# Kernel optimization log

Measured on AMD Instinct MI355X. Metric: run time of the kernel, lower is better.

The kernel has to match this reference:

```python
import jax, jax.numpy as jnp
import numpy as np

N_TRACKS = 2048          # chunk_size = 32*32*2 in the source
CONF_THRESHOLD = 3.0     # conf_threshold default
NORM_INLIER_THRESH = 0.01  # reprojection inlier threshold in normalized camera coords
PIX_THRESH = 1.5         # frame-0 pixel reprojection threshold from the source
MIN_TRI_INLIER = 4       # min_tri_inlier_num default


def setup_inputs() -> dict:
    key = jax.random.key(0)
    k1, k2, k3 = jax.random.split(key, 3)
    S, H, W = 8, 224, 224
    pts = jax.random.normal(k1, (S, H, W, 3), dtype=jnp.float32)
    # confidences in (1, 5) so (conf - 3 + 0.5) weights span negative/positive as in the source
    conf = 1.0 + 4.0 * jax.random.uniform(k2, (S, H, W), dtype=jnp.float32)
    K = jnp.array([[300.0, 0.0, W / 2.0], [0.0, 300.0, H / 2.0], [0.0, 0.0, 1.0]], dtype=jnp.float32)
    intrinsics = jnp.tile(K[None], (S, 1, 1))
    w2cs = jnp.tile(jnp.eye(4, dtype=jnp.float32)[None], (S, 1, 1))
    w2cs = w2cs.at[:, :3, 3].set(0.1 * jax.random.normal(k3, (S, 3), dtype=jnp.float32))
    return {"pts": pts, "conf": conf, "intrinsics": intrinsics, "w2cs": w2cs}


def reference(pts, conf, intrinsics, w2cs):
    S, H, W, _ = pts.shape
    HW = H * W
    pts_flat = pts.reshape(S, HW, 3)
    conf_flat = conf.reshape(S, HW)

    # --- sample N reference points in frame 0 by confidence (fixed-size analogue of quantile mask) ---
    _, idx0 = jax.lax.top_k(conf_flat[0], N_TRACKS)          # [N]
    ref = pts_flat[0, idx0]                                   # [N,3]
    ref_sq = (ref ** 2).sum(-1)                               # [N]

    # --- brute-force pairwise sq-dist + argmin match, per frame (memory-bound core) ---
    def match(frame_pts):  # frame_pts: [HW,3]
        d = ref_sq[:, None] - 2.0 * (ref @ frame_pts.T) + (frame_pts ** 2).sum(-1)[None, :]  # [N,HW]
        return jnp.argmin(d, axis=1)

    matches_rest = jax.lax.map(match, pts_flat[1:])           # [S-1,N]
    matches = jnp.concatenate([idx0[None], matches_rest], 0)  # [S,N]

    xs = (matches % W).astype(pts.dtype)
    ys = (matches // W).astype(pts.dtype)
    track_xy = jnp.stack([xs, ys], -1)                        # [S,N,2] (x,y) per source reorder [...,[1,0]]
    track_conf = jnp.take_along_axis(conf_flat, matches, axis=1)  # [S,N]

    # --- normalize tracks by intrinsics ---
    pp = intrinsics[:, :2, 2][:, None, :]                     # [S,1,2]
    f = jnp.stack([intrinsics[:, 0, 0], intrinsics[:, 1, 1]], -1)[:, None, :]  # [S,1,2]
    tn = (track_xy - pp) / f                                  # [S,N,2]

    # --- weighted multi-view DLT triangulation (conf-weighted, per-point 4x4 eigh) ---
    wgt = track_conf - CONF_THRESHOLD + 0.5                   # [S,N]
    P = w2cs[:, :3, :]                                        # [S,3,4]
    r1 = (tn[..., 0:1] * P[:, None, 2, :] - P[:, None, 0, :]) * wgt[..., None]  # [S,N,4]
    r2 = (tn[..., 1:2] * P[:, None, 2, :] - P[:, None, 1, :]) * wgt[..., None]
    AtA = jnp.einsum('sni,snj->nij', r1, r1) + jnp.einsum('sni,snj->nij', r2, r2)  # [N,4,4]
    _, evecs = jnp.linalg.eigh(AtA)
    v = evecs[..., 0]                                         # eigvec of smallest eigval, [N,4]
    denom = jnp.where(jnp.abs(v[:, 3:4]) < 1e-8, 1e-8, v[:, 3:4])
    X = v[:, :3] / denom                                      # [N,3] triangulated points

    # --- per-view reprojection, inlier count ---
    Xc = jnp.einsum('sij,nj->sni', P[:, :, :3], X) + P[:, None, :, 3]  # [S,N,3]
    z = Xc[..., 2:3]
    z = jnp.where(jnp.abs(z) < 1e-6, 1e-6, z)
    uv = Xc[..., :2] / z                                      # [S,N,2] normalized
    err = jnp.linalg.norm(uv - tn, axis=-1)                   # [S,N]
    inlier = err < NORM_INLIER_THRESH                         # [S,N]
    inlier_num = inlier.sum(0)                                # [N] int32

    # --- frame-0 pixel reprojection mask (source: (pos - track_matches[0]).norm < 1.5 & inlier_num > S//2) ---
    pos = uv[0] * f[0] + pp[0]                                # [N,2] pixels
    err_px0 = jnp.linalg.norm(pos - track_xy[0], axis=-1)
    final_mask = (err_px0 < PIX_THRESH) & (inlier_num > S // 2)

    # --- points_conf as in batched_triangulate ---
    pconf = (track_conf * inlier).sum(0) / jnp.clip(inlier_num, 1)
    pconf = jnp.where(inlier_num >= MIN_TRI_INLIER, pconf, 1.0)

    return X, pconf, final_mask.astype(jnp.int32), inlier_num
```

## Files before the change

kernel.cpp:

```cpp
#include <hip/hip_runtime.h>
#include <math.h>

#define HW       50176
#define W_IMG    224
#define S_FRAMES 8
#define NT       2048
#define NJCH     28
#define JCH      1792

__device__ unsigned           g_hist1[65536];
__device__ unsigned           g_hist2[65536];
__device__ unsigned           g_scalars[16];
__device__ unsigned long long g_keys[4096];
__device__ int                g_matches[S_FRAMES * NT];
__device__ float4             g_ref[NT];
__device__ float              g_pd[7 * NT * NJCH];
__device__ int                g_pj[7 * NT * NJCH];

__device__ __forceinline__ unsigned ordered_u32(float f) {
  unsigned u = __float_as_uint(f);
  return (u & 0x80000000u) ? ~u : (u | 0x80000000u);
}

__global__ void zero_kernel() {
  int i = blockIdx.x * blockDim.x + threadIdx.x;
  if (i < 65536) { g_hist1[i] = 0u; g_hist2[i] = 0u; }
  if (i < 4096)  g_keys[i] = 0ULL;
  if (i < 16)    g_scalars[i] = 0u;
}

__global__ void hist1_kernel(const float* __restrict__ conf) {
  int i = blockIdx.x * blockDim.x + threadIdx.x;
  if (i < HW) atomicAdd(&g_hist1[ordered_u32(conf[i]) >> 16], 1u);
}

__global__ void scan1_kernel() {
  __shared__ unsigned csum[256];
  __shared__ unsigned suf[256];
  int t = threadIdx.x;
  unsigned s = 0;
  for (int b = 0; b < 256; ++b) s += g_hist1[t * 256 + b];
  csum[t] = s;
  __syncthreads();
  if (t == 0) { unsigned run = 0; for (int c = 255; c >= 0; --c) { suf[c] = run; run += csum[c]; } }
  __syncthreads();
  unsigned run = suf[t];
  for (int b = 255; b >= 0; --b) {
    unsigned h = g_hist1[t * 256 + b];
    if (run < NT && run + h >= NT) { g_scalars[0] = (unsigned)(t * 256 + b); g_scalars[1] = run; }
    run += h;
  }
}

__global__ void hist2_kernel(const float* __restrict__ conf) {
  int i = blockIdx.x * blockDim.x + threadIdx.x;
  if (i < HW) {
    unsigned ou = ordered_u32(conf[i]);
    if ((ou >> 16) == g_scalars[0]) atomicAdd(&g_hist2[ou & 0xFFFFu], 1u);
  }
}

__global__ void scan2_kernel() {
  __shared__ unsigned csum[256];
  __shared__ unsigned suf[256];
  int t = threadIdx.x;
  unsigned R = NT - g_scalars[1];
  unsigned s = 0;
  for (int b = 0; b < 256; ++b) s += g_hist2[t * 256 + b];
  csum[t] = s;
  __syncthreads();
  if (t == 0) { unsigned run = 0; for (int c = 255; c >= 0; --c) { suf[c] = run; run += csum[c]; } }
  __syncthreads();
  unsigned run = suf[t];
  for (int b = 255; b >= 0; --b) {
    unsigned h = g_hist2[t * 256 + b];
    if (run < R && run + h >= R) g_scalars[2] = (g_scalars[0] << 16) | (unsigned)(t * 256 + b);
    run += h;
  }
}

__global__ void compact_kernel(const float* __restrict__ conf) {
  int i = blockIdx.x * blockDim.x + threadIdx.x;
  if (i < HW) {
    unsigned ou = ordered_u32(conf[i]);
    if (ou >= g_scalars[2]) {
      unsigned pos = atomicAdd(&g_scalars[4], 1u);
      if (pos < 4096) g_keys[pos] = ((unsigned long long)ou << 32) | (unsigned long long)(0xFFFFFFFFu - (unsigned)i);
    }
  }
}

__global__ __launch_bounds__(1024) void sortwrite_kernel(const float* __restrict__ pts) {
  __shared__ unsigned long long sk[4096];
  int t = threadIdx.x;
  for (int i = t; i < 4096; i += 1024) sk[i] = ~g_keys[i];
  for (unsigned k = 2; k <= 4096; k <<= 1) {
    for (unsigned j = k >> 1; j > 0; j >>= 1) {
      __syncthreads();
      for (unsigned i = t; i < 4096; i += 1024) {
        unsigned ixj = i ^ j;
        if (ixj > i) {
          unsigned long long a = sk[i], b = sk[ixj];
          bool up = ((i & k) == 0);
          if (up ? (a > b) : (a < b)) { sk[i] = b; sk[ixj] = a; }
        }
      }
    }
  }
  __syncthreads();
  for (int i = t; i < NT; i += 1024) {
    unsigned long long key = ~sk[i];
    unsigned idx = 0xFFFFFFFFu - (unsigned)(key & 0xFFFFFFFFu);
    g_matches[i] = (int)idx;
    const float* p = pts + (size_t)idx * 3;
    float x = p[0], y = p[1], z = p[2];
    g_ref[i] = make_float4(x, y, z, fmaf(x, x, fmaf(y, y, z * z)));
  }
}

__global__ __launch_bounds__(256) void match_kernel(const float* __restrict__ pts) {
  __shared__ float4 tile[256];
  int jc = blockIdx.x;
  int ic = blockIdx.y;
  int f  = blockIdx.z;
  int t  = threadIdx.x;
  int i  = ic * 256 + t;
  float4 r = g_ref[i];
  float dmin = INFINITY;
  int   jmin = 0;
  const float* fp = pts + (size_t)(f + 1) * HW * 3;
  int jbase0 = jc * JCH;
  for (int ti = 0; ti < 7; ++ti) {
    int jb = jbase0 + ti * 256;
    const float* p = fp + (size_t)(jb + t) * 3;
    float x = p[0], y = p[1], z = p[2];
    float sq = fmaf(x, x, fmaf(y, y, z * z));
    __syncthreads();
    tile[t] = make_float4(x, y, z, sq);
    __syncthreads();
#pragma unroll 8
    for (int u = 0; u < 256; ++u) {
      float4 q = tile[u];
      float dot = fmaf(q.x, r.x, fmaf(q.y, r.y, q.z * r.z));
      float d   = fmaf(-2.0f, dot, r.w) + q.w;
      if (d < dmin) { dmin = d; jmin = jb + u; }
    }
  }
  int id = f * NT + i;
  g_pd[id * NJCH + jc] = dmin;
  g_pj[id * NJCH + jc] = jmin;
}

__global__ void reduce_kernel() {
  int id = blockIdx.x * blockDim.x + threadIdx.x;
  if (id >= 7 * NT) return;
  float dmin = INFINITY;
  int   jmin = 0;
  for (int c = 0; c < NJCH; ++c) {
    float d = g_pd[id * NJCH + c];
    int   j = g_pj[id * NJCH + c];
    if (d < dmin) { dmin = d; jmin = j; }
  }
  int f = id / NT, i = id % NT;
  g_matches[(f + 1) * NT + i] = jmin;
}

__global__ void solve_kernel(const float* __restrict__ conf, const float* __restrict__ intr,
                             const float* __restrict__ w2cs, float* __restrict__ out) {
  int i = blockIdx.x * blockDim.x + threadIdx.x;
  if (i >= NT) return;

  float A1[10] = {0}, A2[10] = {0};
  float tnx[8], tny[8], cf[8];
  float x0 = 0.f, y0 = 0.f;

  for (int s = 0; s < S_FRAMES; ++s) {
    int m = g_matches[s * NT + i];
    float xs = (float)(m % W_IMG);
    float ys = (float)(m / W_IMG);
    float c  = conf[s * HW + m];
    float fx = intr[s * 9 + 0], fy = intr[s * 9 + 4];
    float cx = intr[s * 9 + 2], cy = intr[s * 9 + 5];
    float tx = (xs - cx) / fx;
    float ty = (ys - cy) / fy;
    float w  = (c - 3.0f) + 0.5f;
    const float* P = w2cs + s * 16;
    float r1[4], r2[4];
#pragma unroll
    for (int k = 0; k < 4; ++k) {
      r1[k] = (tx * P[8 + k] - P[k])     * w;
      r2[k] = (ty * P[8 + k] - P[4 + k]) * w;
    }
    int idx = 0;
#pragma unroll
    for (int a = 0; a < 4; ++a)
#pragma unroll
      for (int b = a; b < 4; ++b) {
        A1[idx] += r1[a] * r1[b];
        A2[idx] += r2[a] * r2[b];
        ++idx;
      }
    tnx[s] = tx; tny[s] = ty; cf[s] = c;
    if (s == 0) { x0 = xs; y0 = ys; }
  }

  double a[4][4], V[4][4];
  {
    int idx = 0;
#pragma unroll
    for (int p = 0; p < 4; ++p)
#pragma unroll
      for (int q = p; q < 4; ++q) {
        double v = (double)(A1[idx] + A2[idx]);
        a[p][q] = v; a[q][p] = v; ++idx;
      }
#pragma unroll
    for (int p = 0; p < 4; ++p)
#pragma unroll
      for (int q = 0; q < 4; ++q) V[p][q] = (p == q) ? 1.0 : 0.0;
  }

  for (int sweep = 0; sweep < 8; ++sweep) {
#pragma unroll
    for (int p = 0; p < 3; ++p)
#pragma unroll
      for (int q = p + 1; q < 4; ++q) {
        double apq = a[p][q];
        if (fabs(apq) <= 1e-40) continue;
        double theta = (a[q][q] - a[p][p]) / (2.0 * apq);
        double tt  = copysign(1.0, theta) / (fabs(theta) + sqrt(theta * theta + 1.0));
        double cth = 1.0 / sqrt(tt * tt + 1.0);
        double sth = tt * cth;
#pragma unroll
        for (int k = 0; k < 4; ++k) {
          double akp = a[p][k], akq = a[q][k];
          a[p][k] = cth * akp - sth * akq;
          a[q][k] = sth * akp + cth * akq;
        }
#pragma unroll
        for (int k = 0; k < 4; ++k) {
          double akp = a[k][p], akq = a[k][q];
          a[k][p] = cth * akp - sth * akq;
          a[k][q] = sth * akp + cth * akq;
        }
#pragma unroll
        for (int k = 0; k < 4; ++k) {
          double vkp = V[k][p], vkq = V[k][q];
          V[k][p] = cth * vkp - sth * vkq;
          V[k][q] = sth * vkp + cth * vkq;
        }
      }
  }

  int kmin = 0; double emin = a[0][0];
#pragma unroll
  for (int k = 1; k < 4; ++k) if (a[k][k] < emin) { emin = a[k][k]; kmin = k; }

  double vsel[4];
#pragma unroll
  for (int r = 0; r < 4; ++r) {
    double x = V[r][0];
    if (kmin == 1) x = V[r][1];
    if (kmin == 2) x = V[r][2];
    if (kmin == 3) x = V[r][3];
    vsel[r] = x;
  }
  float v0 = (float)vsel[0], v1 = (float)vsel[1], v2 = (float)vsel[2], v3 = (float)vsel[3];
  float denom = (fabsf(v3) < 1e-8f) ? 1e-8f : v3;
  float X0 = v0 / denom, X1 = v1 / denom, X2 = v2 / denom;

  int innum = 0; float wsum = 0.f; float u0x = 0.f, u0y = 0.f;
  for (int s = 0; s < S_FRAMES; ++s) {
    const float* P = w2cs + s * 16;
    float Xc0 = fmaf(P[2],  X2, fmaf(P[1], X1, P[0] * X0)) + P[3];
    float Xc1 = fmaf(P[6],  X2, fmaf(P[5], X1, P[4] * X0)) + P[7];
    float z   = fmaf(P[10], X2, fmaf(P[9], X1, P[8] * X0)) + P[11];
    if (fabsf(z) < 1e-6f) z = 1e-6f;
    float ux = Xc0 / z, uy = Xc1 / z;
    float dx = ux - tnx[s], dy = uy - tny[s];
    float e = sqrtf(dx * dx + dy * dy);
    bool in = e < 0.01f;
    if (in) { innum++; wsum += cf[s]; }
    if (s == 0) { u0x = ux; u0y = uy; }
  }
  float fx0 = intr[0], fy0 = intr[4], cx0 = intr[2], cy0 = intr[5];
  float posx = fmaf(u0x, fx0, cx0), posy = fmaf(u0y, fy0, cy0);
  float dxp = posx - x0, dyp = posy - y0;
  float epx = sqrtf(dxp * dxp + dyp * dyp);
  int mask = (epx < 1.5f && innum > 4) ? 1 : 0;
  float pconf = wsum / (float)((innum > 1) ? innum : 1);
  if (innum < 4) pconf = 1.0f;

  out[3 * i + 0] = X0;
  out[3 * i + 1] = X1;
  out[3 * i + 2] = X2;
  out[6144 + i]  = pconf;
  out[8192 + i]  = (float)mask;
  out[10240 + i] = (float)innum;
}

extern "C" void kernel_launch(void* const* d_in, const int* in_sizes, int n_in,
                              void* d_out, int out_size, void* d_ws, size_t ws_size,
                              hipStream_t stream) {
  const float* pts  = (const float*)d_in[0];
  const float* conf = (const float*)d_in[1];
  const float* intr = (const float*)d_in[2];
  const float* w2cs = (const float*)d_in[3];
  float* out = (float*)d_out;

  zero_kernel   <<<256, 256, 0, stream>>>();
  hist1_kernel  <<<196, 256, 0, stream>>>(conf);
  scan1_kernel  <<<1,   256, 0, stream>>>();
  hist2_kernel  <<<196, 256, 0, stream>>>(conf);
  scan2_kernel  <<<1,   256, 0, stream>>>();
  compact_kernel<<<196, 256, 0, stream>>>(conf);
  sortwrite_kernel<<<1, 1024, 0, stream>>>(pts);
  match_kernel  <<<dim3(NJCH, 8, 7), 256, 0, stream>>>(pts);
  reduce_kernel <<<56,  256, 0, stream>>>();
  solve_kernel  <<<32,  64,  0, stream>>>(conf, intr, w2cs, out);
}
```

Before: 418.5 us.

## Register-block four references per thread in match kernel and parallelize histogram scans

The match kernel now has each thread handle four reference points, so every shared-memory tile load feeds four distance computations. It also folds the -2 factor and the squared norm into the tile so each distance is three FMAs. The candidate range is split into 98 chunks of 512 instead of 28 of 1792, which keeps the grid large, but reduce_kernel now has more partials to read. The two scan kernels use 1024 threads with a parallel suffix scan instead of a serial single-thread loop, and the solve launch is reshaped to 8 blocks of 256.

Result: faster. 400.3 us (-4.3%).

```diff
diff --git a/kernel.cpp b/kernel.cpp
--- a/kernel.cpp
+++ b/kernel.cpp
@@ -5,8 +5,9 @@
 #define W_IMG    224
 #define S_FRAMES 8
 #define NT       2048
-#define NJCH     28
-#define JCH      1792
+#define NJCH     98
+#define JCH      512
+#define TPC      2
 
 __device__ unsigned           g_hist1[65536];
 __device__ unsigned           g_hist2[65536];
@@ -34,20 +35,23 @@
   if (i < HW) atomicAdd(&g_hist1[ordered_u32(conf[i]) >> 16], 1u);
 }
 
-__global__ void scan1_kernel() {
-  __shared__ unsigned csum[256];
-  __shared__ unsigned suf[256];
+__global__ __launch_bounds__(1024) void scan1_kernel() {
+  __shared__ unsigned ssum[1024];
   int t = threadIdx.x;
-  unsigned s = 0;
-  for (int b = 0; b < 256; ++b) s += g_hist1[t * 256 + b];
-  csum[t] = s;
+  unsigned mysum = 0;
+  for (int b = 0; b < 64; ++b) mysum += g_hist1[t * 64 + b];
+  ssum[t] = mysum;
   __syncthreads();
-  if (t == 0) { unsigned run = 0; for (int c = 255; c >= 0; --c) { suf[c] = run; run += csum[c]; } }
-  __syncthreads();
-  unsigned run = suf[t];
-  for (int b = 255; b >= 0; --b) {
-    unsigned h = g_hist1[t * 256 + b];
-    if (run < NT && run + h >= NT) { g_scalars[0] = (unsigned)(t * 256 + b); g_scalars[1] = run; }
+  for (int off = 1; off < 1024; off <<= 1) {
+    unsigned v = (t + off < 1024) ? ssum[t + off] : 0u;
+    __syncthreads();
+    ssum[t] += v;
+    __syncthreads();
+  }
+  unsigned run = ssum[t] - mysum;
+  for (int b = 63; b >= 0; --b) {
+    unsigned h = g_hist1[t * 64 + b];
+    if (run < NT && run + h >= NT) { g_scalars[0] = (unsigned)(t * 64 + b); g_scalars[1] = run; }
     run += h;
   }
 }
@@ -60,21 +64,24 @@
   }
 }
 
-__global__ void scan2_kernel() {
-  __shared__ unsigned csum[256];
-  __shared__ unsigned suf[256];
+__global__ __launch_bounds__(1024) void scan2_kernel() {
+  __shared__ unsigned ssum[1024];
   int t = threadIdx.x;
   unsigned R = NT - g_scalars[1];
-  unsigned s = 0;
-  for (int b = 0; b < 256; ++b) s += g_hist2[t * 256 + b];
-  csum[t] = s;
+  unsigned mysum = 0;
+  for (int b = 0; b < 64; ++b) mysum += g_hist2[t * 64 + b];
+  ssum[t] = mysum;
   __syncthreads();
-  if (t == 0) { unsigned run = 0; for (int c = 255; c >= 0; --c) { suf[c] = run; run += csum[c]; } }
-  __syncthreads();
-  unsigned run = suf[t];
-  for (int b = 255; b >= 0; --b) {
-    unsigned h = g_hist2[t * 256 + b];
-    if (run < R && run + h >= R) g_scalars[2] = (g_scalars[0] << 16) | (unsigned)(t * 256 + b);
+  for (int off = 1; off < 1024; off <<= 1) {
+    unsigned v = (t + off < 1024) ? ssum[t + off] : 0u;
+    __syncthreads();
+    ssum[t] += v;
+    __syncthreads();
+  }
+  unsigned run = ssum[t] - mysum;
+  for (int b = 63; b >= 0; --b) {
+    unsigned h = g_hist2[t * 64 + b];
+    if (run < R && run + h >= R) g_scalars[2] = (g_scalars[0] << 16) | (unsigned)(t * 64 + b);
     run += h;
   }
 }
@@ -124,31 +131,44 @@
   int ic = blockIdx.y;
   int f  = blockIdx.z;
   int t  = threadIdx.x;
-  int i  = ic * 256 + t;
-  float4 r = g_ref[i];
-  float dmin = INFINITY;
-  int   jmin = 0;
+  int ib = ic * 1024 + t;
+
+  float4 r0 = g_ref[ib];
+  float4 r1 = g_ref[ib + 256];
+  float4 r2 = g_ref[ib + 512];
+  float4 r3 = g_ref[ib + 768];
+  float dmin0 = INFINITY, dmin1 = INFINITY, dmin2 = INFINITY, dmin3 = INFINITY;
+  int   jmin0 = 0, jmin1 = 0, jmin2 = 0, jmin3 = 0;
+
   const float* fp = pts + (size_t)(f + 1) * HW * 3;
   int jbase0 = jc * JCH;
-  for (int ti = 0; ti < 7; ++ti) {
+  for (int ti = 0; ti < TPC; ++ti) {
     int jb = jbase0 + ti * 256;
     const float* p = fp + (size_t)(jb + t) * 3;
     float x = p[0], y = p[1], z = p[2];
     float sq = fmaf(x, x, fmaf(y, y, z * z));
     __syncthreads();
-    tile[t] = make_float4(x, y, z, sq);
-    __syncthreads();
-#pragma unroll 8
+    tile[t] = make_float4(-2.0f * x, -2.0f * y, -2.0f * z, sq);
+    __syncthreads();
+#pragma unroll 4
     for (int u = 0; u < 256; ++u) {
       float4 q = tile[u];
-      float dot = fmaf(q.x, r.x, fmaf(q.y, r.y, q.z * r.z));
-      float d   = fmaf(-2.0f, dot, r.w) + q.w;
-      if (d < dmin) { dmin = d; jmin = jb + u; }
+      int ju = jb + u;
+      float d0 = fmaf(q.x, r0.x, fmaf(q.y, r0.y, fmaf(q.z, r0.z, q.w)));
+      float d1 = fmaf(q.x, r1.x, fmaf(q.y, r1.y, fmaf(q.z, r1.z, q.w)));
+      float d2 = fmaf(q.x, r2.x, fmaf(q.y, r2.y, fmaf(q.z, r2.z, q.w)));
+      float d3 = fmaf(q.x, r3.x, fmaf(q.y, r3.y, fmaf(q.z, r3.z, q.w)));
+      if (d0 < dmin0) { dmin0 = d0; jmin0 = ju; }
+      if (d1 < dmin1) { dmin1 = d1; jmin1 = ju; }
+      if (d2 < dmin2) { dmin2 = d2; jmin2 = ju; }
+      if (d3 < dmin3) { dmin3 = d3; jmin3 = ju; }
     }
   }
-  int id = f * NT + i;
-  g_pd[id * NJCH + jc] = dmin;
-  g_pj[id * NJCH + jc] = jmin;
+  int id0 = f * NT + ib;
+  g_pd[(id0)       * NJCH + jc] = dmin0;  g_pj[(id0)       * NJCH + jc] = jmin0;
+  g_pd[(id0 + 256) * NJCH + jc] = dmin1;  g_pj[(id0 + 256) * NJCH + jc] = jmin1;
+  g_pd[(id0 + 512) * NJCH + jc] = dmin2;  g_pj[(id0 + 512) * NJCH + jc] = jmin2;
+  g_pd[(id0 + 768) * NJCH + jc] = dmin3;  g_pj[(id0 + 768) * NJCH + jc] = jmin3;
 }
 
 __global__ void reduce_kernel() {
@@ -310,12 +330,12 @@
 
   zero_kernel   <<<256, 256, 0, stream>>>();
   hist1_kernel  <<<196, 256, 0, stream>>>(conf);
-  scan1_kernel  <<<1,   256, 0, stream>>>();
+  scan1_kernel  <<<1,  1024, 0, stream>>>();
   hist2_kernel  <<<196, 256, 0, stream>>>(conf);
-  scan2_kernel  <<<1,   256, 0, stream>>>();
+  scan2_kernel  <<<1,  1024, 0, stream>>>();
   compact_kernel<<<196, 256, 0, stream>>>(conf);
   sortwrite_kernel<<<1, 1024, 0, stream>>>(pts);
-  match_kernel  <<<dim3(NJCH, 8, 7), 256, 0, stream>>>(pts);
+  match_kernel  <<<dim3(NJCH, 2, 7), 256, 0, stream>>>(pts);
   reduce_kernel <<<56,  256, 0, stream>>>();
-  solve_kernel  <<<32,  64,  0, stream>>>(conf, intr, w2cs, out);
-}
+  solve_kernel  <<<8,  256, 0, stream>>>(conf, intr, w2cs, out);
+}
```
